# Optimization experiments

Measured on AMD Instinct MI355X. Metric: run time of the kernel, lower is better.

The kernel has to match this reference:

```python
import jax, jax.numpy as jnp
import numpy as np

B, S, D = 2, 2048, 1024
H = 16
DK = D // H


def setup_inputs() -> dict:
    key = jax.random.key(0)
    ks = jax.random.split(key, 5)
    std = np.sqrt(2.0 / (D + D))
    x = jax.random.normal(ks[0], (B, S, D), dtype=jnp.float32)
    wq = jax.random.normal(ks[1], (D, D), dtype=jnp.float32) * std
    wk = jax.random.normal(ks[2], (D, D), dtype=jnp.float32) * std
    wv = jax.random.normal(ks[3], (D, D), dtype=jnp.float32) * std
    wo = jax.random.normal(ks[4], (D, D), dtype=jnp.float32) * std
    return {"x": x, "wq": wq, "wk": wk, "wv": wv, "wo": wo}


def reference(x, wq, wk, wv, wo):
    # Linear: y = x @ W.T  (weight stored as [d_out, d_in])
    q = jnp.einsum("bsd,ed->bse", x, wq)
    k = jnp.einsum("bsd,ed->bse", x, wk)
    v = jnp.einsum("bsd,ed->bse", x, wv)
    # split heads: [B, S, H*DK] -> [B, H, S, DK]
    q = q.reshape(B, S, H, DK).transpose(0, 2, 1, 3)
    k = k.reshape(B, S, H, DK).transpose(0, 2, 1, 3)
    v = v.reshape(B, S, H, DK).transpose(0, 2, 1, 3)
    scale = 1.0 / jnp.sqrt(jnp.asarray(DK, dtype=x.dtype))
    scores = jnp.einsum("bhqd,bhkd->bhqk", q, k) * scale  # [B,H,S,S]
    causal = jnp.tril(jnp.ones((S, S), dtype=bool))
    scores = jnp.where(causal, scores, -jnp.inf)
    attn = jax.nn.softmax(scores, axis=-1)
    out = jnp.einsum("bhqk,bhkd->bhqd", attn, v)  # [B,H,S,DK]
    out = out.transpose(0, 2, 1, 3).reshape(B, S, D)
    return jnp.einsum("bsd,ed->bse", out, wo)
```

## Files before the change

### kernel.cpp

```cpp
#include <hip/hip_runtime.h>
#include <hip/hip_bf16.h>
#include <cstdint>

#define B_ 2
#define S_ 2048
#define D_ 1024
#define H_ 16
#define DK_ 64

#define LOG2E_S 0.18033688f

typedef __attribute__((ext_vector_type(8))) short bf16x8;
typedef __attribute__((ext_vector_type(4))) float f32x4;

__device__ __forceinline__ unsigned short f2bf(float f) {
  unsigned u = __float_as_uint(f);
  u = (u + 0x7FFFu + ((u >> 16) & 1u)) >> 16;
  return (unsigned short)u;
}

__device__ __forceinline__ unsigned short f2bf_hw(float f) {
  __hip_bfloat16 h = __float2bfloat16(f);
  return *reinterpret_cast<unsigned short*>(&h);
}

typedef __attribute__((address_space(1))) void gv_t;
typedef __attribute__((address_space(3))) void lv_t;
__device__ __forceinline__ void gl16(const void* g, void* l) {
  __builtin_amdgcn_global_load_lds((gv_t*)g, (lv_t*)l, 16, 0, 0);
}

__device__ __forceinline__ void stage8w(const unsigned short* gbase, size_t ldg,
                                        unsigned short* lds, int wave, int lane) {
  const int lr = lane >> 3;
  const int col8 = (lane & 7) ^ lr;
  gl16(gbase + (size_t)(wave * 8 + lr) * ldg + col8 * 8, lds + wave * 512);
}

__device__ __forceinline__ bf16x8 rdswz(const unsigned short* lds, int row, int col) {
  return *(const bf16x8*)&lds[row * 64 + (col ^ ((row & 7) << 3))];
}

__global__ void cvt_all_kernel(const float* __restrict__ x,
                               const float* __restrict__ w0, const float* __restrict__ w1,
                               const float* __restrict__ w2, const float* __restrict__ w3,
                               unsigned short* __restrict__ xo,
                               unsigned short* __restrict__ o0, unsigned short* __restrict__ o1,
                               unsigned short* __restrict__ o2, unsigned short* __restrict__ o3) {
  const int mat = blockIdx.y;
  const float* in = (mat == 0) ? x : (mat == 1) ? w0 : (mat == 2) ? w1 : (mat == 3) ? w2 : w3;
  unsigned short* out = (mat == 0) ? xo : (mat == 1) ? o0 : (mat == 2) ? o1 : (mat == 3) ? o2 : o3;
  const int n4 = (mat == 0) ? (B_ * S_ * D_ / 4) : (D_ * D_ / 4);
  int i = blockIdx.x * blockDim.x + threadIdx.x;
  if (i >= n4) return;
  const float4 v = reinterpret_cast<const float4*>(in)[i];
  ushort4 o;
  o.x = f2bf(v.x); o.y = f2bf(v.y); o.z = f2bf(v.z); o.w = f2bf(v.w);
  reinterpret_cast<ushort4*>(out)[i] = o;
}

#define BM 128
#define BK 64

template <typename OutT, bool TV2, int BNv, bool SCALEQ>
__global__ __launch_bounds__(256) void gemm_bt(
    const unsigned short* __restrict__ A,
    const unsigned short* __restrict__ B0, const unsigned short* __restrict__ B1,
    const unsigned short* __restrict__ B2,
    OutT* __restrict__ C0, OutT* __restrict__ C1, OutT* __restrict__ C2,
    int M, int N, int K) {
  constexpr int NFRAG = BNv / 32;
  __shared__ unsigned short lA[BM * BK];
  __shared__ unsigned short lB[BNv * BK];
  const int tid = threadIdx.x;
  const int wave = tid >> 6, lane = tid & 63;
  const int l16 = lane & 15, lqq = lane >> 4;
  const int wr = wave >> 1, wc = wave & 1;
  const int lr = lane >> 3;
  const int col8 = ((lane & 7) ^ lr) * 8;

  const int tilesPerMat = N / BNv;
  const int bx = blockIdx.x;
  const int mat = bx / tilesPerMat;
  const int n0 = (bx % tilesPerMat) * BNv;
  const unsigned short* Bm = (mat == 0) ? B0 : (mat == 1) ? B1 : B2;
  OutT* C = (mat == 0) ? C0 : (mat == 1) ? C1 : C2;
  const int m0 = blockIdx.y * BM;

  f32x4 acc[4][NFRAG] = {};

  for (int k0 = 0; k0 < K; k0 += BK) {
    __syncthreads();
#pragma unroll
    for (int c = wave; c < 16; c += 4)
      gl16(A + (size_t)(m0 + c * 8 + lr) * K + k0 + col8, &lA[c * 512]);
#pragma unroll
    for (int c = wave; c < BNv / 8; c += 4)
      gl16(Bm + (size_t)(n0 + c * 8 + lr) * K + k0 + col8, &lB[c * 512]);
    __syncthreads();
#pragma unroll
    for (int kk = 0; kk < BK / 32; ++kk) {
      bf16x8 af[4], bfr[NFRAG];
#pragma unroll
      for (int m = 0; m < 4; ++m)
        af[m] = rdswz(lA, wr * 64 + m * 16 + l16, kk * 32 + lqq * 8);
#pragma unroll
      for (int n = 0; n < NFRAG; ++n)
        bfr[n] = rdswz(lB, wc * (BNv / 2) + n * 16 + l16, kk * 32 + lqq * 8);
      __builtin_amdgcn_s_setprio(1);
#pragma unroll
      for (int m = 0; m < 4; ++m)
#pragma unroll
        for (int n = 0; n < NFRAG; ++n)
          acc[m][n] = __builtin_amdgcn_mfma_f32_16x16x32_bf16(af[m], bfr[n], acc[m][n], 0, 0, 0);
      __builtin_amdgcn_s_setprio(0);
    }
  }

  if (TV2 && mat == 2) {
    unsigned short* Vt = (unsigned short*)C;
#pragma unroll
    for (int m = 0; m < 4; ++m)
#pragma unroll
      for (int n = 0; n < NFRAG; ++n) {
        int r0 = m0 + wr * 64 + m * 16 + lqq * 4;
        int cidx = n0 + wc * (BNv / 2) + n * 16 + l16;
        int bb = r0 >> 11, s = r0 & 2047;
        int h = cidx >> 6, dv = cidx & 63;
        ushort4 o;
        o.x = f2bf(acc[m][n][0]); o.y = f2bf(acc[m][n][1]);
        o.z = f2bf(acc[m][n][2]); o.w = f2bf(acc[m][n][3]);
        *(ushort4*)(Vt + ((size_t)((bb * H_ + h) * DK_ + dv)) * S_ + s) = o;
      }
  } else {
    const float cscale = (SCALEQ && mat == 0) ? LOG2E_S : 1.0f;
#pragma unroll
    for (int m = 0; m < 4; ++m)
#pragma unroll
      for (int n = 0; n < NFRAG; ++n)
#pragma unroll
        for (int j = 0; j < 4; ++j) {
          int r = m0 + wr * 64 + m * 16 + lqq * 4 + j;
          int cidx = n0 + wc * (BNv / 2) + n * 16 + l16;
          float v = acc[m][n][j] * cscale;
          if constexpr (sizeof(OutT) == 4) C[(size_t)r * N + cidx] = v;
          else C[(size_t)r * N + cidx] = f2bf(v);
        }
  }
}

__global__ __launch_bounds__(512) void attn_kernel(
    const unsigned short* __restrict__ Qg, const unsigned short* __restrict__ Kg,
    const unsigned short* __restrict__ Vtg, unsigned short* __restrict__ Og) {
  __shared__ unsigned short sQ[2][64 * 64];
  __shared__ unsigned short sK[2][64 * 64];
  __shared__ unsigned short sVt[2][64 * 64];
  __shared__ unsigned short sP[8][2][16 * 64];
  const int tid = threadIdx.x, wave = tid >> 6, lane = tid & 63;
  const int side = wave >> 2, wq = wave & 3;
  const int l16 = lane & 15, lq = lane >> 4;
  const int id = blockIdx.x;
  const int bh = (id & 7) * 4 + ((id >> 3) & 3);
  const int g = (id >> 5) & 7;
  const int i = (id < 256) ? (15 - g) : g;
  const int b = bh >> 4, h = bh & 15;
  const int qtA = 2 * i, qtB = 2 * i + 1;
  const int qt_s = side ? qtB : qtA;
  const int NT = i + 1;
  const size_t tokbase = (size_t)b * S_ * D_ + h * DK_;
  const unsigned short* VtB = Vtg + (size_t)(b * H_ + h) * DK_ * S_;
  unsigned short (*sPw)[16 * 64] = sP[wave];

  stage8w(Qg + tokbase + (size_t)(qtA * 64) * D_, D_, sQ[0], wave, lane);
  stage8w(Qg + tokbase + (size_t)(qtB * 64) * D_, D_, sQ[1], wave, lane);
  __syncthreads();
  bf16x8 aq0 = rdswz(sQ[side], wq * 16 + l16, lq * 8);
  bf16x8 aq1 = rdswz(sQ[side], wq * 16 + l16, 32 + lq * 8);

  const float THR2 = 11.5416f;
  const short ONE_BF = 0x3F80;
  const bf16x8 vones = {ONE_BF, ONE_BF, ONE_BF, ONE_BF, ONE_BF, ONE_BF, ONE_BF, ONE_BF};
  float m_run[4] = {-1e30f, -1e30f, -1e30f, -1e30f};
  f32x4 sum_acc = {};
  f32x4 o_acc[4] = {};

#pragma unroll 1
  for (int kt = 0; kt < NT; ++kt) {
    __syncthreads();
    stage8w(Kg + tokbase + (size_t)(kt * 128) * D_, D_, sK[0], wave, lane);
    stage8w(Kg + tokbase + (size_t)(kt * 128 + 64) * D_, D_, sK[1], wave, lane);
    stage8w(VtB + kt * 128, S_, sVt[0], wave, lane);
    stage8w(VtB + kt * 128 + 64, S_, sVt[1], wave, lane);
    __syncthreads();

    const bool last = (kt == NT - 1);
    float p[8][4];

#pragma unroll
    for (int sub = 0; sub < 2; ++sub) {
      const bool skip = (sub == 1) && (side == 0) && last;
      if (!skip) {
        __builtin_amdgcn_s_setprio(1);
#pragma unroll
        for (int nb = 0; nb < 4; ++nb) {
          bf16x8 bk0 = rdswz(sK[sub], nb * 16 + l16, lq * 8);
          bf16x8 bk1 = rdswz(sK[sub], nb * 16 + l16, 32 + lq * 8);
          f32x4 a = {};
          a = __builtin_amdgcn_mfma_f32_16x16x32_bf16(aq0, bk0, a, 0, 0, 0);
          a = __builtin_amdgcn_mfma_f32_16x16x32_bf16(aq1, bk1, a, 0, 0, 0);
#pragma unroll
          for (int j = 0; j < 4; ++j) p[sub * 4 + nb][j] = a[j];
        }
        __builtin_amdgcn_s_setprio(0);
      } else {
#pragma unroll
        for (int nb = 0; nb < 4; ++nb)
#pragma unroll
          for (int j = 0; j < 4; ++j) p[sub * 4 + nb][j] = -1e30f;
      }
    }

    if (last) {
      if (side == 0) {
#pragma unroll
        for (int nb = 0; nb < 4; ++nb)
#pragma unroll
          for (int j = 0; j < 4; ++j) {
            int kidx = nb * 16 + l16;
            int qidx = wq * 16 + lq * 4 + j;
            if (kidx > qidx) p[nb][j] = -1e30f;
          }
      } else {
#pragma unroll
        for (int nb = 0; nb < 4; ++nb)
#pragma unroll
          for (int j = 0; j < 4; ++j) {
            int kidx = nb * 16 + l16;
            int qidx = wq * 16 + lq * 4 + j;
            if (kidx > qidx) p[4 + nb][j] = -1e30f;
          }
      }
    }

    float pmax[4];
    bool ok = true;
#pragma unroll
    for (int j = 0; j < 4; ++j) {
      float r = p[0][j];
#pragma unroll
      for (int nbb = 1; nbb < 8; ++nbb) r = fmaxf(r, p[nbb][j]);
      pmax[j] = r;
      ok = ok && (r <= m_run[j] + THR2);
    }
    if (!__all((int)ok)) {
#pragma unroll
      for (int j = 0; j < 4; ++j) {
        float r = pmax[j];
#pragma unroll
        for (int d = 1; d < 16; d <<= 1) r = fmaxf(r, __shfl_xor(r, d));
        float mn = fmaxf(m_run[j], r);
        float alpha = exp2f(m_run[j] - mn);
        m_run[j] = mn;
        sum_acc[j] *= alpha;
#pragma unroll
        for (int nb = 0; nb < 4; ++nb) o_acc[nb][j] *= alpha;
      }
    }
#pragma unroll
    for (int j = 0; j < 4; ++j) {
      const int rw = lq * 4 + j;
#pragma unroll
      for (int nbb = 0; nbb < 8; ++nbb) {
        float e = exp2f(p[nbb][j] - m_run[j]);
        sPw[nbb >> 2][rw * 64 + (((nbb & 3) * 16 + l16) ^ ((rw & 7) << 3))] = f2bf_hw(e);
      }
    }

    __builtin_amdgcn_s_setprio(1);
#pragma unroll
    for (int sub = 0; sub < 2; ++sub)
#pragma unroll
      for (int kk = 0; kk < 2; ++kk) {
        bf16x8 ap = rdswz(sPw[sub], l16, kk * 32 + lq * 8);
        sum_acc = __builtin_amdgcn_mfma_f32_16x16x32_bf16(ap, vones, sum_acc, 0, 0, 0);
#pragma unroll
        for (int nb = 0; nb < 4; ++nb) {
          bf16x8 bv = rdswz(sVt[sub], nb * 16 + l16, kk * 32 + lq * 8);
          o_acc[nb] = __builtin_amdgcn_mfma_f32_16x16x32_bf16(ap, bv, o_acc[nb], 0, 0, 0);
        }
      }
    __builtin_amdgcn_s_setprio(0);
  }

#pragma unroll
  for (int j = 0; j < 4; ++j) {
    float inv = 1.f / sum_acc[j];
#pragma unroll
    for (int nb = 0; nb < 4; ++nb) {
      int r = qt_s * 64 + wq * 16 + lq * 4 + j;
      Og[tokbase + (size_t)r * D_ + nb * 16 + l16] = f2bf(o_acc[nb][j] * inv);
    }
  }
}

extern "C" void kernel_launch(void* const* d_in, const int* in_sizes, int n_in,
                              void* d_out, int out_size, void* d_ws, size_t ws_size,
                              hipStream_t stream) {
  const float* x = (const float*)d_in[0];
  const float* wq = (const float*)d_in[1];
  const float* wk = (const float*)d_in[2];
  const float* wv = (const float*)d_in[3];
  const float* wo = (const float*)d_in[4];
  float* out = (float*)d_out;

  char* ws = (char*)d_ws;
  const size_t MB = 1024 * 1024;
  unsigned short* xb  = (unsigned short*)(ws + 0);
  unsigned short* wqb = (unsigned short*)(ws + 8 * MB);
  unsigned short* wkb = (unsigned short*)(ws + 10 * MB);
  unsigned short* wvb = (unsigned short*)(ws + 12 * MB);
  unsigned short* wob = (unsigned short*)(ws + 14 * MB);
  unsigned short* Qb  = (unsigned short*)(ws + 16 * MB);
  unsigned short* Kb  = (unsigned short*)(ws + 24 * MB);
  unsigned short* Vtb = (unsigned short*)(ws + 32 * MB);
  unsigned short* AOb = (unsigned short*)(ws + 40 * MB);

  const int M = B_ * S_;
  const int N = D_, K = D_;

  cvt_all_kernel<<<dim3(B_ * S_ * D_ / 4 / 256, 5), 256, 0, stream>>>(
      x, wq, wk, wv, wo, xb, wqb, wkb, wvb, wob);

  gemm_bt<unsigned short, true, 128, true><<<dim3(3 * (N / 128), M / BM), 256, 0, stream>>>(
      xb, wqb, wkb, wvb, Qb, Kb, Vtb, M, N, K);

  attn_kernel<<<dim3(512), 512, 0, stream>>>(Qb, Kb, Vtb, AOb);

  gemm_bt<float, false, 64, false><<<dim3(N / 64, M / BM), 256, 0, stream>>>(
      AOb, wob, wob, wob, out, out, out, M, N, K);
}
```

Before: 111.2 us.

## Double-buffer K/V tiles in attention kernel and alias Q staging onto P buffer

Adds double-buffered shared memory for K and V^T so the next tile's loads are issued before computing on the current tile, replacing two barriers per iteration with one. Q is staged temporarily in the sP scratch region to keep the LDS footprint down despite the doubled K/V buffers. The intent is to overlap global-to-LDS staging latency with MFMA work; the risk is that stage8w is synchronous, so overlap depends on how the compiler schedules it, and LDS use rises, which can lower occupancy.

New measurement: 123.3 us. +10.9%, slower.

```diff
diff --git a/kernel.cpp b/kernel.cpp
--- a/kernel.cpp
+++ b/kernel.cpp
@@ -152,9 +152,8 @@
 __global__ __launch_bounds__(512) void attn_kernel(
     const unsigned short* __restrict__ Qg, const unsigned short* __restrict__ Kg,
     const unsigned short* __restrict__ Vtg, unsigned short* __restrict__ Og) {
-  __shared__ unsigned short sQ[2][64 * 64];
-  __shared__ unsigned short sK[2][64 * 64];
-  __shared__ unsigned short sVt[2][64 * 64];
+  __shared__ unsigned short sKb[2][2][64 * 64];
+  __shared__ unsigned short sVtb[2][2][64 * 64];
   __shared__ unsigned short sP[8][2][16 * 64];
   const int tid = threadIdx.x, wave = tid >> 6, lane = tid & 63;
   const int side = wave >> 2, wq = wave & 3;
@@ -170,12 +169,18 @@
   const size_t tokbase = (size_t)b * S_ * D_ + h * DK_;
   const unsigned short* VtB = Vtg + (size_t)(b * H_ + h) * DK_ * S_;
   unsigned short (*sPw)[16 * 64] = sP[wave];
-
-  stage8w(Qg + tokbase + (size_t)(qtA * 64) * D_, D_, sQ[0], wave, lane);
-  stage8w(Qg + tokbase + (size_t)(qtB * 64) * D_, D_, sQ[1], wave, lane);
+  unsigned short* sPflat = &sP[0][0][0];
+
+  stage8w(Qg + tokbase + (size_t)(qtA * 64) * D_, D_, sPflat, wave, lane);
+  stage8w(Qg + tokbase + (size_t)(qtB * 64) * D_, D_, sPflat + 4096, wave, lane);
+  stage8w(Kg + tokbase, D_, sKb[0][0], wave, lane);
+  stage8w(Kg + tokbase + (size_t)64 * D_, D_, sKb[0][1], wave, lane);
+  stage8w(VtB, S_, sVtb[0][0], wave, lane);
+  stage8w(VtB + 64, S_, sVtb[0][1], wave, lane);
   __syncthreads();
-  bf16x8 aq0 = rdswz(sQ[side], wq * 16 + l16, lq * 8);
-  bf16x8 aq1 = rdswz(sQ[side], wq * 16 + l16, 32 + lq * 8);
+  bf16x8 aq0 = rdswz(sPflat + side * 4096, wq * 16 + l16, lq * 8);
+  bf16x8 aq1 = rdswz(sPflat + side * 4096, wq * 16 + l16, 32 + lq * 8);
+  __syncthreads();
 
   const float THR2 = 11.5416f;
   const short ONE_BF = 0x3F80;
@@ -186,12 +191,13 @@
 
 #pragma unroll 1
   for (int kt = 0; kt < NT; ++kt) {
-    __syncthreads();
-    stage8w(Kg + tokbase + (size_t)(kt * 128) * D_, D_, sK[0], wave, lane);
-    stage8w(Kg + tokbase + (size_t)(kt * 128 + 64) * D_, D_, sK[1], wave, lane);
-    stage8w(VtB + kt * 128, S_, sVt[0], wave, lane);
-    stage8w(VtB + kt * 128 + 64, S_, sVt[1], wave, lane);
-    __syncthreads();
+    const int cur = kt & 1;
+    if (kt + 1 < NT) {
+      stage8w(Kg + tokbase + (size_t)((kt + 1) * 128) * D_, D_, sKb[cur ^ 1][0], wave, lane);
+      stage8w(Kg + tokbase + (size_t)((kt + 1) * 128 + 64) * D_, D_, sKb[cur ^ 1][1], wave, lane);
+      stage8w(VtB + (kt + 1) * 128, S_, sVtb[cur ^ 1][0], wave, lane);
+      stage8w(VtB + (kt + 1) * 128 + 64, S_, sVtb[cur ^ 1][1], wave, lane);
+    }
 
     const bool last = (kt == NT - 1);
     float p[8][4];
@@ -203,8 +209,8 @@
         __builtin_amdgcn_s_setprio(1);
 #pragma unroll
         for (int nb = 0; nb < 4; ++nb) {
-          bf16x8 bk0 = rdswz(sK[sub], nb * 16 + l16, lq * 8);
-          bf16x8 bk1 = rdswz(sK[sub], nb * 16 + l16, 32 + lq * 8);
+          bf16x8 bk0 = rdswz(sKb[cur][sub], nb * 16 + l16, lq * 8);
+          bf16x8 bk1 = rdswz(sKb[cur][sub], nb * 16 + l16, 32 + lq * 8);
           f32x4 a = {};
           a = __builtin_amdgcn_mfma_f32_16x16x32_bf16(aq0, bk0, a, 0, 0, 0);
           a = __builtin_amdgcn_mfma_f32_16x16x32_bf16(aq1, bk1, a, 0, 0, 0);
@@ -285,11 +291,13 @@
         sum_acc = __builtin_amdgcn_mfma_f32_16x16x32_bf16(ap, vones, sum_acc, 0, 0, 0);
 #pragma unroll
         for (int nb = 0; nb < 4; ++nb) {
-          bf16x8 bv = rdswz(sVt[sub], nb * 16 + l16, kk * 32 + lq * 8);
+          bf16x8 bv = rdswz(sVtb[cur][sub], nb * 16 + l16, kk * 32 + lq * 8);
           o_acc[nb] = __builtin_amdgcn_mfma_f32_16x16x32_bf16(ap, bv, o_acc[nb], 0, 0, 0);
         }
       }
     __builtin_amdgcn_s_setprio(0);
+
+    __syncthreads();
   }
 
 #pragma unroll
```
